# Kernel tuning notes

Hardware: AMD Instinct MI355X
Metric: run time of the kernel (lower is better)

The kernel has to match this reference:

```python
import jax, jax.numpy as jnp
import numpy as np
from jax import lax

B, T, N, FIN = 1, 8, 50000, 3
E = 800000
HID, HEADS = 32, 2
NEG_SLOPE = 0.2  # PyG GATConv default negative_slope


def setup_inputs() -> dict:
    key = jax.random.key(0)
    ks = jax.random.split(key, 16)
    p = lambda k, shape: jax.random.normal(k, shape, dtype=jnp.float32) * 0.1
    return {
        "x_seq": jax.random.normal(ks[0], (B, T, N, FIN), dtype=jnp.float32),
        # GAT layer 1: lin weight [heads*hid, in], att vectors [heads, hid], bias [hid]
        "W1": p(ks[1], (HEADS * HID, FIN)),
        "a1_src": p(ks[2], (HEADS, HID)),
        "a1_dst": p(ks[3], (HEADS, HID)),
        "b1": p(ks[4], (HID,)),
        # GAT layer 2
        "W2": p(ks[5], (HEADS * HID, HID)),
        "a2_src": p(ks[6], (HEADS, HID)),
        "a2_dst": p(ks[7], (HEADS, HID)),
        "b2": p(ks[8], (HID,)),
        # GRU (single layer): torch layout [3*hid, hid] with gate order r,z,n
        "w_ih": p(ks[9], (3 * HID, HID)),
        "w_hh": p(ks[10], (3 * HID, HID)),
        "b_ih": p(ks[11], (3 * HID,)),
        "b_hh": p(ks[12], (3 * HID,)),
        # final Linear(hid, 1)
        "fc_w": p(ks[13], (1, HID)),
        "fc_b": p(ks[14], (1,)),
        "edge_index": jax.random.randint(ks[15], (2, E), 0, N, dtype=jnp.int64),
    }


def gat(x, src, dst, W, a_s, a_d, b):
    """PyG GATConv, heads=HEADS, concat=False (mean over heads). src/dst include self-loops."""
    n = x.shape[0]
    heads, hd = a_s.shape
    h = (x @ W.T).reshape(n, heads, hd)                      # [n, heads, hid]
    e = jax.nn.leaky_relu((h * a_s).sum(-1)[src] + (h * a_d).sum(-1)[dst], NEG_SLOPE)  # [E', heads]
    m = jax.ops.segment_max(e, dst, num_segments=n)          # per-destination max
    m = jnp.where(jnp.isfinite(m), m, jnp.zeros_like(m))
    ex = jnp.exp(e - m[dst])
    denom = jax.ops.segment_sum(ex, dst, num_segments=n)
    alpha = ex / (denom[dst] + 1e-16)                        # segment softmax
    out = jax.ops.segment_sum(h[src] * alpha[..., None], dst, num_segments=n)  # [n, heads, hid]
    return out.mean(axis=1) + b


def _forward(x_seq, W1, a1_src, a1_dst, b1, W2, a2_src, a2_dst, b2,
             w_ih, w_hh, b_ih, b_hh, fc_w, fc_b, edge_index):
    Bb, Tt, Nn, Fin = x_seq.shape
    n = Bb * Nn
    loops = jnp.arange(n, dtype=edge_index.dtype)            # add_self_loops=True
    src = jnp.concatenate([edge_index[0], loops])
    dst = jnp.concatenate([edge_index[1], loops])
    hid = b1.shape[0]

    def step(hstate, xt):                                    # one timestep: GAT x2 then GRU cell
        x = xt.reshape(n, Fin)
        g = jax.nn.relu(gat(x, src, dst, W1, a1_src, a1_dst, b1))
        g = jax.nn.relu(gat(g, src, dst, W2, a2_src, a2_dst, b2))
        gi = g @ w_ih.T + b_ih
        gh = hstate @ w_hh.T + b_hh
        i_r, i_z, i_n = jnp.split(gi, 3, axis=-1)
        h_r, h_z, h_n = jnp.split(gh, 3, axis=-1)
        r = jax.nn.sigmoid(i_r + h_r)
        z = jax.nn.sigmoid(i_z + h_z)
        cand = jnp.tanh(i_n + r * h_n)
        hnew = (1.0 - z) * cand + z * hstate
        return hnew, None

    h0 = jnp.zeros((n, hid), x_seq.dtype)
    h_final, _ = lax.scan(step, h0, jnp.moveaxis(x_seq, 1, 0))  # scan over T
    out = h_final @ fc_w.T + fc_b                            # [B*N, 1]
    return out.reshape(Bb, Nn)


def reference(x_seq, W1, a1_src, a1_dst, b1, W2, a2_src, a2_dst, b2,
              w_ih, w_hh, b_ih, b_hh, fc_w, fc_b, edge_index):
    return _forward(x_seq, W1, a1_src, a1_dst, b1, W2, a2_src, a2_dst, b2,
                    w_ih, w_hh, b_ih, b_hh, fc_w, fc_b, edge_index)
```

## Files before the change

kernel.cpp:

```cpp
#include <hip/hip_runtime.h>
#include <hip/hip_fp16.h>
#include <stdint.h>

#define T_STEPS 8
#define FIN 3
#define HID 32
#define NEG_SLOPE 0.2f
#define LOG2E 1.4426950408889634f

typedef __fp16 v4h __attribute__((ext_vector_type(4)));
typedef float  v4f __attribute__((ext_vector_type(4)));

__device__ __forceinline__ float lrelu(float x) { return x > 0.f ? x : NEG_SLOPE * x; }
__device__ __forceinline__ float sigmoidf(float x) { return 1.f / (1.f + __expf(-x)); }

__global__ void detect_kernel(const int* ei32, int nElems, int* flag) {
    __shared__ int any_nonzero;
    if (threadIdx.x == 0) any_nonzero = 0;
    __syncthreads();
    int idx = 1 + 2 * (int)threadIdx.x;
    if (idx < nElems && ei32[idx] != 0) any_nonzero = 1;
    __syncthreads();
    if (threadIdx.x == 0) *flag = (any_nonzero ? 0 : 1);
}

__device__ __forceinline__ int get_edge(const void* ei, int is64, long long idx) {
    if (is64) return (int)((const long long*)ei)[idx];
    return ((const int*)ei)[idx];
}

__global__ void init_kernel(int* cnt, int N) {
    int i = blockIdx.x * 256 + threadIdx.x;
    if (i < N) cnt[i] = 1;
}

__global__ void conv_count_kernel(const void* ei, const int* flag, int E, int N,
                                  int* src32, int* dst32, int* cnt) {
    int e = blockIdx.x * 256 + threadIdx.x;
    if (e >= E) return;
    int is64 = *flag;
    int s = get_edge(ei, is64, e);
    int d = get_edge(ei, is64, (long long)E + e);
    if ((unsigned)s >= (unsigned)N) s = 0;
    src32[e] = s;
    int dd = ((unsigned)d < (unsigned)N) ? d : 0x7fffffff;
    dst32[e] = dd;
    if (dd < N) atomicAdd(&cnt[dd], 1);
}

__global__ __launch_bounds__(256) void scan1_kernel(const int* cnt, int* rowptr, int* bsum, int n) {
    __shared__ int sm[256];
    int i = blockIdx.x * 256 + threadIdx.x;
    int v = (i < n) ? cnt[i] : 0;
    sm[threadIdx.x] = v;
    __syncthreads();
    for (int off = 1; off < 256; off <<= 1) {
        int t = (threadIdx.x >= off) ? sm[threadIdx.x - off] : 0;
        __syncthreads();
        sm[threadIdx.x] += t;
        __syncthreads();
    }
    if (i < n) rowptr[i + 1] = sm[threadIdx.x];
    if (threadIdx.x == 255) bsum[blockIdx.x] = sm[255];
}

__global__ __launch_bounds__(256) void scan2_kernel(int* bsum, int nb) {
    __shared__ int sm[256];
    int v = (threadIdx.x < nb) ? bsum[threadIdx.x] : 0;
    sm[threadIdx.x] = v;
    __syncthreads();
    for (int off = 1; off < 256; off <<= 1) {
        int t = (threadIdx.x >= off) ? sm[threadIdx.x - off] : 0;
        __syncthreads();
        sm[threadIdx.x] += t;
        __syncthreads();
    }
    if (threadIdx.x < nb) bsum[threadIdx.x] = sm[threadIdx.x];
}

__global__ __launch_bounds__(256) void scan3_kernel(int* rowptr, const int* bsum, int n) {
    int i = blockIdx.x * 256 + threadIdx.x;
    if (i < n && blockIdx.x > 0) rowptr[i + 1] += bsum[blockIdx.x - 1];
    if (i == 0) rowptr[0] = 0;
}

__global__ void selffill_kernel(const int* rowptr, int* csr, int* fill, int N) {
    int n = blockIdx.x * 256 + threadIdx.x;
    if (n >= N) return;
    int rp = rowptr[n];
    csr[rp] = n;
    fill[n] = rp + 1;
}

__global__ void scatter_kernel(const int* __restrict__ src32, const int* __restrict__ dst32,
                               int E, int lo, int hi, int* fill, int* csr) {
    int e = blockIdx.x * 256 + threadIdx.x;
    if (e >= E) return;
    int d = dst32[e];
    if (d < lo || d >= hi) return;
    int p = atomicAdd(&fill[d], 1);
    csr[p] = src32[e];
}

__global__ __launch_bounds__(64) void prep_u_kernel(
        const float* __restrict__ W2, const float* __restrict__ a2s,
        const float* __restrict__ a2d, float* __restrict__ u_s, float* __restrict__ u_d) {
    int l = threadIdx.x;
    int h = l >> 5, k = l & 31;
    float us = 0.f, ud = 0.f;
    for (int c = 0; c < 32; c++) {
        float w = W2[(h * 32 + c) * 32 + k];
        us += a2s[h * 32 + c] * w;
        ud += a2d[h * 32 + c] * w;
    }
    u_s[l] = us * LOG2E;
    u_d[l] = ud * LOG2E;
}

__global__ __launch_bounds__(256) void packfrag_kernel(
        const float* __restrict__ W2, const float* __restrict__ w_ih,
        const float* __restrict__ w_hh, uint2* __restrict__ wfrag) {
    int idx = blockIdx.x * 256 + threadIdx.x;
    if (idx >= 2048) return;
    int tile = idx >> 6, l = idx & 63;
    int c = l & 15, g = l >> 4;
    float v[4];
    if (tile < 8) {
        int kt = tile >> 1, nt = tile & 1;
#pragma unroll
        for (int b = 0; b < 4; b++) {
            int kk = kt * 16 + 4 * g + b;
            int nn = nt * 16 + c;
            v[b] = 0.5f * (kk < 32 ? W2[nn * 32 + kk] : W2[(nn + 32) * 32 + kk - 32]);
        }
    } else if (tile < 20) {
        int q = tile - 8; int nt = q >> 1, kt = q & 1;
#pragma unroll
        for (int b = 0; b < 4; b++) {
            int kk = kt * 16 + 4 * g + b;
            int nn = nt * 16 + c;
            v[b] = w_ih[nn * 32 + kk];
        }
    } else {
        int q = tile - 20; int nt = q >> 1, kt = q & 1;
#pragma unroll
        for (int b = 0; b < 4; b++) {
            int kk = kt * 16 + 4 * g + b;
            int nn = nt * 16 + c;
            v[b] = w_hh[nn * 32 + kk];
        }
    }
    __half2 lo = __floats2half2_rn(v[0], v[1]);
    __half2 hi = __floats2half2_rn(v[2], v[3]);
    uint2 u;
    u.x = *(unsigned*)&lo;
    u.y = *(unsigned*)&hi;
    wfrag[tile * 64 + l] = u;
}

__global__ __launch_bounds__(256) void score1_all(
        const float* __restrict__ x_seq, const float* __restrict__ W1,
        const float* __restrict__ a1s, const float* __restrict__ a1d,
        float4* __restrict__ nrec4, float2* __restrict__ sd1, int N) {
    int t = blockIdx.x;
    int node = blockIdx.y * 256 + threadIdx.x;
    if (node >= N) return;
    const float* xp = x_seq + ((size_t)t * N + node) * FIN;
    float x0 = xp[0], x1 = xp[1], x2 = xp[2];
    float ps0 = 0.f, ps1 = 0.f, pd0 = 0.f, pd1 = 0.f;
    for (int c = 0; c < 32; c++) {
        float h0 = W1[c * 3] * x0 + W1[c * 3 + 1] * x1 + W1[c * 3 + 2] * x2;
        float h1 = W1[96 + c * 3] * x0 + W1[97 + c * 3] * x1 + W1[98 + c * 3] * x2;
        ps0 += h0 * a1s[c]; pd0 += h0 * a1d[c];
        ps1 += h1 * a1s[32 + c]; pd1 += h1 * a1d[32 + c];
    }
    ps0 *= LOG2E; ps1 *= LOG2E; pd0 *= LOG2E; pd1 *= LOG2E;
    unsigned u = (unsigned)__half_as_ushort(__float2half_rn(ps0)) |
                 ((unsigned)__half_as_ushort(__float2half_rn(ps1)) << 16);
    float4 r;
    r.x = x0; r.y = x1; r.z = x2; r.w = __uint_as_float(u);
    nrec4[(size_t)t * N + node] = r;
    sd1[(size_t)t * N + node] = make_float2(pd0, pd1);
}

__device__ __forceinline__ void unpack_scores(float wslot, float& s0, float& s1) {
    unsigned u = __float_as_uint(wslot);
    s0 = __half2float(__ushort_as_half((unsigned short)(u & 0xffffu)));
    s1 = __half2float(__ushort_as_half((unsigned short)(u >> 16)));
}

__global__ __launch_bounds__(64) void aggA_all(
        const int* __restrict__ rowptr, const int* __restrict__ csr,
        const float4* __restrict__ nrec4, const float2* __restrict__ sd1,
        const float* __restrict__ W1, const float* __restrict__ b1,
        const float* __restrict__ u_s, const float* __restrict__ u_d,
        __half2* __restrict__ g1h, float2* __restrict__ ssd2, float2* __restrict__ sd2, int N) {
    int t = blockIdx.x;
    int dst = blockIdx.y * 64 + threadIdx.x;
    if (dst >= N) return;
    const float4* nr = nrec4 + (size_t)t * N;
    int rs = rowptr[dst], re = rowptr[dst + 1];
    float2 sdv = sd1[(size_t)t * N + dst];
    float q0 = 0, qx0 = 0, qx1 = 0, qx2 = 0;
    float q1 = 0, qy0 = 0, qy1 = 0, qy2 = 0;
#define AGGA_EDGE(rr) { \
        float s0h, s1h; unpack_scores(rr.w, s0h, s1h); \
        float w0 = exp2f(lrelu(s0h + sdv.x)); \
        float w1 = exp2f(lrelu(s1h + sdv.y)); \
        q0 += w0; qx0 += w0 * rr.x; qx1 += w0 * rr.y; qx2 += w0 * rr.z; \
        q1 += w1; qy0 += w1 * rr.x; qy1 += w1 * rr.y; qy2 += w1 * rr.z; }
    int e = rs;
    for (; e + 4 <= re; e += 4) {
        int s0 = csr[e], s1 = csr[e + 1], s2 = csr[e + 2], s3 = csr[e + 3];
        float4 r0 = nr[s0], r1 = nr[s1], r2 = nr[s2], r3 = nr[s3];
        AGGA_EDGE(r0); AGGA_EDGE(r1); AGGA_EDGE(r2); AGGA_EDGE(r3);
    }
    for (; e < re; e++) {
        float4 r = nr[csr[e]];
        AGGA_EDGE(r);
    }
#undef AGGA_EDGE
    float inv0 = 1.f / (q0 + 1e-16f), inv1 = 1.f / (q1 + 1e-16f);
    float ax0 = qx0 * inv0, ax1 = qx1 * inv0, ax2 = qx2 * inv0;
    float ay0 = qy0 * inv1, ay1 = qy1 * inv1, ay2 = qy2 * inv1;
    float ps0 = 0, ps1 = 0, pd0 = 0, pd1 = 0;
    float4 out[4];
    __half2* ghp = (__half2*)out;
    float gprev = 0.f;
#pragma unroll
    for (int c = 0; c < 32; c++) {
        float v0 = W1[c * 3] * ax0 + W1[c * 3 + 1] * ax1 + W1[c * 3 + 2] * ax2;
        float v1 = W1[96 + c * 3] * ay0 + W1[97 + c * 3] * ay1 + W1[98 + c * 3] * ay2;
        float g = fmaxf(0.5f * (v0 + v1) + b1[c], 0.f);
        ps0 += g * u_s[c];      ps1 += g * u_s[32 + c];
        pd0 += g * u_d[c];      pd1 += g * u_d[32 + c];
        if (c & 1) ghp[c >> 1] = __floats2half2_rn(gprev, g);
        else gprev = g;
    }
    float4* gdst = (float4*)(g1h + (size_t)t * N * 16 + (size_t)dst * 16);
    gdst[0] = out[0]; gdst[1] = out[1]; gdst[2] = out[2]; gdst[3] = out[3];
    ssd2[(size_t)t * N + dst] = make_float2(ps0, ps1);
    sd2[(size_t)t * N + dst]  = make_float2(pd0, pd1);
}

__global__ __launch_bounds__(256) void aggBg_all(
        const int* __restrict__ rowptr, const int* __restrict__ csr,
        const __half2* __restrict__ g1h,
        const float2* __restrict__ ssd2, const float2* __restrict__ sd2,
        __half2* __restrict__ aggH, int N) {
    int t = blockIdx.x;
    int dl = threadIdx.x >> 2;
    int q = threadIdx.x & 3;
    int dst = blockIdx.y * 64 + dl;
    if (dst >= N) return;
    const __half2* gbase = g1h + (size_t)t * N * 16 + q * 4;
    const float2* ss = ssd2 + (size_t)t * N;
    int rs = rowptr[dst], re = rowptr[dst + 1];
    float2 sdv = sd2[(size_t)t * N + dst];
    float a0[8] = {0, 0, 0, 0, 0, 0, 0, 0};
    float a1[8] = {0, 0, 0, 0, 0, 0, 0, 0};
    float den0 = 0.f, den1 = 0.f;
#define AGGB_EDGE(sc, gv) { \
        float w0 = exp2f(lrelu(sc.x + sdv.x)); \
        float w1 = exp2f(lrelu(sc.y + sdv.y)); \
        den0 += w0; den1 += w1; \
        float2 p0 = __half22float2(*(const __half2*)&gv.x); \
        float2 p1 = __half22float2(*(const __half2*)&gv.y); \
        float2 p2 = __half22float2(*(const __half2*)&gv.z); \
        float2 p3 = __half22float2(*(const __half2*)&gv.w); \
        a0[0] += w0 * p0.x; a0[1] += w0 * p0.y; a0[2] += w0 * p1.x; a0[3] += w0 * p1.y; \
        a0[4] += w0 * p2.x; a0[5] += w0 * p2.y; a0[6] += w0 * p3.x; a0[7] += w0 * p3.y; \
        a1[0] += w1 * p0.x; a1[1] += w1 * p0.y; a1[2] += w1 * p1.x; a1[3] += w1 * p1.y; \
        a1[4] += w1 * p2.x; a1[5] += w1 * p2.y; a1[6] += w1 * p3.x; a1[7] += w1 * p3.y; }
    int e = rs;
    for (; e + 4 <= re; e += 4) {
        int s0 = csr[e], s1 = csr[e + 1], s2 = csr[e + 2], s3 = csr[e + 3];
        float2 c0 = ss[s0], c1 = ss[s1], c2 = ss[s2], c3 = ss[s3];
        float4 g0 = *(const float4*)(gbase + (size_t)s0 * 16);
        float4 g1 = *(const float4*)(gbase + (size_t)s1 * 16);
        float4 g2 = *(const float4*)(gbase + (size_t)s2 * 16);
        float4 g3 = *(const float4*)(gbase + (size_t)s3 * 16);
        AGGB_EDGE(c0, g0); AGGB_EDGE(c1, g1); AGGB_EDGE(c2, g2); AGGB_EDGE(c3, g3);
    }
    for (; e < re; e++) {
        int s = csr[e];
        float2 c = ss[s];
        float4 g = *(const float4*)(gbase + (size_t)s * 16);
        AGGB_EDGE(c, g);
    }
#undef AGGB_EDGE
    float i0 = 1.f / (den0 + 1e-16f), i1 = 1.f / (den1 + 1e-16f);
    __half2 o0[4], o1[4];
#pragma unroll
    for (int j = 0; j < 4; j++) {
        o0[j] = __floats2half2_rn(a0[2 * j] * i0, a0[2 * j + 1] * i0);
        o1[j] = __floats2half2_rn(a1[2 * j] * i1, a1[2 * j + 1] * i1);
    }
    __half2* row = aggH + (size_t)t * N * 32 + (size_t)dst * 32;
    *(float4*)(row + q * 4)      = *(float4*)o0;
    *(float4*)(row + 16 + q * 4) = *(float4*)o1;
}

__global__ __launch_bounds__(64) void gru_mfma(
        const __half2* __restrict__ aggH, const uint2* __restrict__ wfrag,
        const float* __restrict__ b2, const float* __restrict__ b_ih,
        const float* __restrict__ b_hh, const float* __restrict__ fc_w,
        const float* __restrict__ fc_b, float* __restrict__ out, int N) {
    __shared__ __align__(16) __half g_lds[16 * 36];
    __shared__ __align__(16) __half h_lds[16 * 36];
    int l = threadIdx.x;
    int c = l & 15;
    int g4 = l >> 4;
    int node0 = blockIdx.x * 16;
    union FU { uint2 u; v4h h; };
    v4h Bw2[4][2], Bih[6][2], Bhh[6][2];
#pragma unroll
    for (int kt = 0; kt < 4; kt++)
#pragma unroll
        for (int nt = 0; nt < 2; nt++) {
            FU f; f.u = wfrag[(kt * 2 + nt) * 64 + l]; Bw2[kt][nt] = f.h;
        }
#pragma unroll
    for (int nt = 0; nt < 6; nt++)
#pragma unroll
        for (int kt = 0; kt < 2; kt++) {
            FU f; f.u = wfrag[(8 + nt * 2 + kt) * 64 + l]; Bih[nt][kt] = f.h;
            f.u = wfrag[(20 + nt * 2 + kt) * 64 + l]; Bhh[nt][kt] = f.h;
        }
    float b2v0 = b2[c], b2v1 = b2[c + 16];
    float bir0 = b_ih[c], bir1 = b_ih[c + 16];
    float biz0 = b_ih[32 + c], biz1 = b_ih[48 + c];
    float bin0 = b_ih[64 + c], bin1 = b_ih[80 + c];
    float bhr0 = b_hh[c], bhr1 = b_hh[c + 16];
    float bhz0 = b_hh[32 + c], bhz1 = b_hh[48 + c];
    float bhn0 = b_hh[64 + c], bhn1 = b_hh[80 + c];
    float fcw0 = fc_w[c], fcw1 = fc_w[c + 16];
    v4f hold0 = {0.f, 0.f, 0.f, 0.f};
    v4f hold1 = {0.f, 0.f, 0.f, 0.f};
    const __half2* rowb = aggH + (size_t)(node0 + c) * 32;
    for (int t = 0; t < T_STEPS; t++) {
        v4f Dg0 = {0.f, 0.f, 0.f, 0.f}, Dg1 = {0.f, 0.f, 0.f, 0.f};
        const __half2* rb = rowb + (size_t)t * N * 32;
#pragma unroll
        for (int kt = 0; kt < 4; kt++) {
            FU A; A.u = *(const uint2*)(rb + 2 * g4 + 8 * kt);
            Dg0 = __builtin_amdgcn_mfma_f32_16x16x16f16(A.h, Bw2[kt][0], Dg0, 0, 0, 0);
            Dg1 = __builtin_amdgcn_mfma_f32_16x16x16f16(A.h, Bw2[kt][1], Dg1, 0, 0, 0);
        }
        __syncthreads();
#pragma unroll
        for (int i = 0; i < 4; i++) {
            int nrow = 4 * g4 + i;
            g_lds[nrow * 36 + c]      = __float2half_rn(fmaxf(Dg0[i] + b2v0, 0.f));
            g_lds[nrow * 36 + c + 16] = __float2half_rn(fmaxf(Dg1[i] + b2v1, 0.f));
        }
        __syncthreads();
        v4f Di[6], Dh[6];
#pragma unroll
        for (int nt = 0; nt < 6; nt++) { Di[nt] = {0.f, 0.f, 0.f, 0.f}; Dh[nt] = {0.f, 0.f, 0.f, 0.f}; }
#pragma unroll
        for (int kt = 0; kt < 2; kt++) {
            FU Ag; Ag.u = *(const uint2*)&g_lds[c * 36 + 4 * g4 + 16 * kt];
#pragma unroll
            for (int nt = 0; nt < 6; nt++)
                Di[nt] = __builtin_amdgcn_mfma_f32_16x16x16f16(Ag.h, Bih[nt][kt], Di[nt], 0, 0, 0);
        }
        if (t > 0) {
#pragma unroll
            for (int kt = 0; kt < 2; kt++) {
                FU Ah; Ah.u = *(const uint2*)&h_lds[c * 36 + 4 * g4 + 16 * kt];
#pragma unroll
                for (int nt = 0; nt < 6; nt++)
                    Dh[nt] = __builtin_amdgcn_mfma_f32_16x16x16f16(Ah.h, Bhh[nt][kt], Dh[nt], 0, 0, 0);
            }
        }
        v4f hn0, hn1;
#pragma unroll
        for (int i = 0; i < 4; i++) {
            {
                float rr = sigmoidf((Di[0][i] + bir0) + (Dh[0][i] + bhr0));
                float zz = sigmoidf((Di[2][i] + biz0) + (Dh[2][i] + bhz0));
                float cand = tanhf((Di[4][i] + bin0) + rr * (Dh[4][i] + bhn0));
                hn0[i] = (1.f - zz) * cand + zz * hold0[i];
            }
            {
                float rr = sigmoidf((Di[1][i] + bir1) + (Dh[1][i] + bhr1));
                float zz = sigmoidf((Di[3][i] + biz1) + (Dh[3][i] + bhz1));
                float cand = tanhf((Di[5][i] + bin1) + rr * (Dh[5][i] + bhn1));
                hn1[i] = (1.f - zz) * cand + zz * hold1[i];
            }
        }
        hold0 = hn0; hold1 = hn1;
        if (t < T_STEPS - 1) {
            __syncthreads();
#pragma unroll
            for (int i = 0; i < 4; i++) {
                int nrow = 4 * g4 + i;
                h_lds[nrow * 36 + c]      = __float2half_rn(hn0[i]);
                h_lds[nrow * 36 + c + 16] = __float2half_rn(hn1[i]);
            }
            __syncthreads();
        }
    }
#pragma unroll
    for (int i = 0; i < 4; i++) {
        float p = fcw0 * hold0[i] + fcw1 * hold1[i];
        p += __shfl_xor(p, 1, 64);
        p += __shfl_xor(p, 2, 64);
        p += __shfl_xor(p, 4, 64);
        p += __shfl_xor(p, 8, 64);
        if (c == 0) out[node0 + 4 * g4 + i] = p + fc_b[0];
    }
}

extern "C" void kernel_launch(void* const* d_in, const int* in_sizes, int n_in,
                              void* d_out, int out_size, void* d_ws, size_t ws_size,
                              hipStream_t stream) {
    const float* x_seq = (const float*)d_in[0];
    const float* W1  = (const float*)d_in[1];
    const float* a1s = (const float*)d_in[2];
    const float* a1d = (const float*)d_in[3];
    const float* b1  = (const float*)d_in[4];
    const float* W2  = (const float*)d_in[5];
    const float* a2s = (const float*)d_in[6];
    const float* a2d = (const float*)d_in[7];
    const float* b2  = (const float*)d_in[8];
    const float* w_ih = (const float*)d_in[9];
    const float* w_hh = (const float*)d_in[10];
    const float* b_ih = (const float*)d_in[11];
    const float* b_hh = (const float*)d_in[12];
    const float* fc_w = (const float*)d_in[13];
    const float* fc_b = (const float*)d_in[14];
    const void*  ei   = d_in[15];

    const int N = in_sizes[0] / (T_STEPS * FIN);
    const int E = in_sizes[15] / 2;
    const int NE = E + N;
    const int NB = (N + 255) / 256;
    const int NB64 = (N + 63) / 64;
    const int NB16 = (N + 15) / 16;
    const int EB = (E + 255) / 256;

    char* ws = (char*)d_ws;
    size_t off = 0;
    auto alloc = [&](size_t bytes) -> void* {
        void* p = ws + off;
        off += (bytes + 255) & ~(size_t)255;
        return p;
    };
    int*     flag   = (int*)alloc(4);
    int*     rowptr = (int*)alloc((size_t)(N + 1) * 4);
    int*     cnt    = (int*)alloc((size_t)N * 4);
    int*     bsum   = (int*)alloc(256 * 4);
    int*     csr    = (int*)alloc((size_t)NE * 4);
    int*     src32  = (int*)alloc((size_t)E * 4);
    int*     dst32  = (int*)alloc((size_t)E * 4);
    float4*  nrec4  = (float4*)alloc((size_t)T_STEPS * N * 16);
    float2*  sd1    = (float2*)alloc((size_t)T_STEPS * N * 8);
    float2*  ssd2   = (float2*)alloc((size_t)T_STEPS * N * 8);
    float2*  sd2    = (float2*)alloc((size_t)T_STEPS * N * 8);
    __half2* g1h    = (__half2*)alloc((size_t)T_STEPS * N * 16 * 4);
    __half2* aggH   = (__half2*)alloc((size_t)T_STEPS * N * 32 * 4);
    float*   u_s    = (float*)alloc(64 * 4);
    float*   u_d    = (float*)alloc(64 * 4);
    uint2*   wfrag  = (uint2*)alloc(32 * 64 * 8);
    if (off > ws_size) return;

    detect_kernel<<<1, 128, 0, stream>>>((const int*)ei, in_sizes[15], flag);
    init_kernel<<<NB, 256, 0, stream>>>(cnt, N);
    conv_count_kernel<<<EB, 256, 0, stream>>>(ei, flag, E, N, src32, dst32, cnt);
    scan1_kernel<<<NB, 256, 0, stream>>>(cnt, rowptr, bsum, N);
    scan2_kernel<<<1, 256, 0, stream>>>(bsum, NB);
    scan3_kernel<<<NB, 256, 0, stream>>>(rowptr, bsum, N);
    selffill_kernel<<<NB, 256, 0, stream>>>(rowptr, csr, cnt, N);
    {
        const int NPASS = 4;
        int per = (N + NPASS - 1) / NPASS;
        for (int p = 0; p < NPASS; p++) {
            int lo = p * per;
            int hi = min(lo + per, N);
            scatter_kernel<<<EB, 256, 0, stream>>>(src32, dst32, E, lo, hi, cnt, csr);
        }
    }
    prep_u_kernel<<<1, 64, 0, stream>>>(W2, a2s, a2d, u_s, u_d);
    packfrag_kernel<<<8, 256, 0, stream>>>(W2, w_ih, w_hh, wfrag);

    score1_all<<<dim3(T_STEPS, NB), 256, 0, stream>>>(x_seq, W1, a1s, a1d, nrec4, sd1, N);
    aggA_all<<<dim3(T_STEPS, NB64), 64, 0, stream>>>(rowptr, csr, nrec4, sd1, W1, b1,
                                                     u_s, u_d, g1h, ssd2, sd2, N);
    aggBg_all<<<dim3(T_STEPS, NB64), 256, 0, stream>>>(rowptr, csr, g1h, ssd2, sd2, aggH, N);
    gru_mfma<<<NB16, 64, 0, stream>>>(aggH, wfrag, b2, b_ih, b_hh,
                                      fc_w, fc_b, (float*)d_out, N);
}
```

Measured before the change: 290.4 us.

## Fuse layer-2 W2 projection into aggregation kernel, shrink GRU input buffer

Moves the layer-2 GAT linear projection (W2 matmul, head mean, bias, ReLU) out of the GRU MFMA kernel into the aggregation kernel. Aggregated features are staged in LDS and multiplied by a transposed fp32 W2 using scalar FMAs. The kernel then writes a 32-wide fp16 g2 instead of the 64-wide aggH. This halves the intermediate buffer written and read between kernels and removes two LDS syncs per timestep from the GRU loop. In exchange the projection runs on vector ALUs instead of MFMA, and the aggregation kernel gains a barrier and LDS use.

```diff
diff --git a/kernel.cpp b/kernel.cpp
--- a/kernel.cpp
+++ b/kernel.cpp
@@ -117,45 +117,38 @@
     u_d[l] = ud * LOG2E;
 }
 
+__global__ __launch_bounds__(256) void pack_kernel(
+        const float* __restrict__ W2, float* __restrict__ w2pk) {
+    int idx = blockIdx.x * 256 + threadIdx.x;
+    if (idx < 2048) {
+        int k = idx >> 6, c = idx & 63;
+        w2pk[idx] = W2[c * 32 + k];
+    }
+}
+
 __global__ __launch_bounds__(256) void packfrag_kernel(
-        const float* __restrict__ W2, const float* __restrict__ w_ih,
-        const float* __restrict__ w_hh, uint2* __restrict__ wfrag) {
+        const float* __restrict__ w_ih, const float* __restrict__ w_hh,
+        uint2* __restrict__ wfrag) {
     int idx = blockIdx.x * 256 + threadIdx.x;
-    if (idx >= 2048) return;
-    int tile = idx >> 6, l = idx & 63;
+    if (idx >= 1536) return;
+    int q24 = idx >> 6, l = idx & 63;
     int c = l & 15, g = l >> 4;
+    const float* W = (q24 < 12) ? w_ih : w_hh;
+    int q = (q24 < 12) ? q24 : q24 - 12;
+    int nt = q >> 1, kt = q & 1;
     float v[4];
-    if (tile < 8) {
-        int kt = tile >> 1, nt = tile & 1;
-#pragma unroll
-        for (int b = 0; b < 4; b++) {
-            int kk = kt * 16 + 4 * g + b;
-            int nn = nt * 16 + c;
-            v[b] = 0.5f * (kk < 32 ? W2[nn * 32 + kk] : W2[(nn + 32) * 32 + kk - 32]);
-        }
-    } else if (tile < 20) {
-        int q = tile - 8; int nt = q >> 1, kt = q & 1;
-#pragma unroll
-        for (int b = 0; b < 4; b++) {
-            int kk = kt * 16 + 4 * g + b;
-            int nn = nt * 16 + c;
-            v[b] = w_ih[nn * 32 + kk];
-        }
-    } else {
-        int q = tile - 20; int nt = q >> 1, kt = q & 1;
-#pragma unroll
-        for (int b = 0; b < 4; b++) {
-            int kk = kt * 16 + 4 * g + b;
-            int nn = nt * 16 + c;
-            v[b] = w_hh[nn * 32 + kk];
-        }
+#pragma unroll
+    for (int b = 0; b < 4; b++) {
+        int kk = kt * 16 + 4 * g + b;
+        int nn = nt * 16 + c;
+        v[b] = W[nn * 32 + kk];
     }
     __half2 lo = __floats2half2_rn(v[0], v[1]);
     __half2 hi = __floats2half2_rn(v[2], v[3]);
     uint2 u;
     u.x = *(unsigned*)&lo;
     u.y = *(unsigned*)&hi;
-    wfrag[tile * 64 + l] = u;
+    wfrag[(8 + q24) * 64 + l] = u;
 }
 
 __global__ __launch_bounds__(256) void score1_all(
@@ -243,23 +236,27 @@
     sd2[(size_t)t * N + dst]  = make_float2(pd0, pd1);
 }
 
-__global__ __launch_bounds__(256) void aggBg_all(
+__global__ __launch_bounds__(256) void aggBg2_all(
         const int* __restrict__ rowptr, const int* __restrict__ csr,
         const __half2* __restrict__ g1h,
         const float2* __restrict__ ssd2, const float2* __restrict__ sd2,
-        __half2* __restrict__ aggH, int N) {
+        const float* __restrict__ w2pk, const float* __restrict__ b2,
+        __half2* __restrict__ g2H, int N) {
+    __shared__ __half2 a_lds[64 * 33];
     int t = blockIdx.x;
-    int dl = threadIdx.x >> 2;
-    int q = threadIdx.x & 3;
-    int dst = blockIdx.y * 64 + dl;
-    if (dst >= N) return;
-    const __half2* gbase = g1h + (size_t)t * N * 16 + q * 4;
-    const float2* ss = ssd2 + (size_t)t * N;
-    int rs = rowptr[dst], re = rowptr[dst + 1];
-    float2 sdv = sd2[(size_t)t * N + dst];
-    float a0[8] = {0, 0, 0, 0, 0, 0, 0, 0};
-    float a1[8] = {0, 0, 0, 0, 0, 0, 0, 0};
-    float den0 = 0.f, den1 = 0.f;
+    int tid = threadIdx.x;
+    int node0 = blockIdx.y * 64;
+    int dl = tid >> 2;
+    int q = tid & 3;
+    int dst = node0 + dl;
+    if (dst < N) {
+        const __half2* gbase = g1h + (size_t)t * N * 16 + q * 4;
+        const float2* ss = ssd2 + (size_t)t * N;
+        int rs = rowptr[dst], re = rowptr[dst + 1];
+        float2 sdv = sd2[(size_t)t * N + dst];
+        float a0[8] = {0, 0, 0, 0, 0, 0, 0, 0};
+        float a1[8] = {0, 0, 0, 0, 0, 0, 0, 0};
+        float den0 = 0.f, den1 = 0.f;
 #define AGGB_EDGE(sc, gv) { \
         float w0 = exp2f(lrelu(sc.x + sdv.x)); \
         float w1 = exp2f(lrelu(sc.y + sdv.y)); \
@@ -272,54 +269,67 @@
         a0[4] += w0 * p2.x; a0[5] += w0 * p2.y; a0[6] += w0 * p3.x; a0[7] += w0 * p3.y; \
         a1[0] += w1 * p0.x; a1[1] += w1 * p0.y; a1[2] += w1 * p1.x; a1[3] += w1 * p1.y; \
         a1[4] += w1 * p2.x; a1[5] += w1 * p2.y; a1[6] += w1 * p3.x; a1[7] += w1 * p3.y; }
-    int e = rs;
-    for (; e + 4 <= re; e += 4) {
-        int s0 = csr[e], s1 = csr[e + 1], s2 = csr[e + 2], s3 = csr[e + 3];
-        float2 c0 = ss[s0], c1 = ss[s1], c2 = ss[s2], c3 = ss[s3];
-        float4 g0 = *(const float4*)(gbase + (size_t)s0 * 16);
-        float4 g1 = *(const float4*)(gbase + (size_t)s1 * 16);
-        float4 g2 = *(const float4*)(gbase + (size_t)s2 * 16);
-        float4 g3 = *(const float4*)(gbase + (size_t)s3 * 16);
-        AGGB_EDGE(c0, g0); AGGB_EDGE(c1, g1); AGGB_EDGE(c2, g2); AGGB_EDGE(c3, g3);
-    }
-    for (; e < re; e++) {
-        int s = csr[e];
-        float2 c = ss[s];
-        float4 g = *(const float4*)(gbase + (size_t)s * 16);
-        AGGB_EDGE(c, g);
-    }
+        int e = rs;
+        for (; e + 4 <= re; e += 4) {
+            int s0 = csr[e], s1 = csr[e + 1], s2 = csr[e + 2], s3 = csr[e + 3];
+            float2 c0 = ss[s0], c1 = ss[s1], c2 = ss[s2], c3 = ss[s3];
+            float4 g0 = *(const float4*)(gbase + (size_t)s0 * 16);
+            float4 g1 = *(const float4*)(gbase + (size_t)s1 * 16);
+            float4 g2 = *(const float4*)(gbase + (size_t)s2 * 16);
+            float4 g3 = *(const float4*)(gbase + (size_t)s3 * 16);
+            AGGB_EDGE(c0, g0); AGGB_EDGE(c1, g1); AGGB_EDGE(c2, g2); AGGB_EDGE(c3, g3);
+        }
+        for (; e < re; e++) {
+            int s = csr[e];
+            float2 c = ss[s];
+            float4 g = *(const float4*)(gbase + (size_t)s * 16);
+            AGGB_EDGE(c, g);
+        }
 #undef AGGB_EDGE
-    float i0 = 1.f / (den0 + 1e-16f), i1 = 1.f / (den1 + 1e-16f);
-    __half2 o0[4], o1[4];
+        float i0 = 1.f / (den0 + 1e-16f), i1 = 1.f / (den1 + 1e-16f);
+#pragma unroll
+        for (int j = 0; j < 4; j++) {
+            a_lds[dl * 33 + q * 4 + j]      = __floats2half2_rn(a0[2 * j] * i0, a0[2 * j + 1] * i0);
+            a_lds[dl * 33 + 16 + q * 4 + j] = __floats2half2_rn(a1[2 * j] * i1, a1[2 * j + 1] * i1);
+        }
+    }
+    __syncthreads();
+    int nl = tid & 63;
+    int cg8 = __builtin_amdgcn_readfirstlane((tid >> 6) * 8);
+    int node = node0 + nl;
+    if (node >= N) return;
+    float acc[8] = {0, 0, 0, 0, 0, 0, 0, 0};
+    for (int kp = 0; kp < 16; kp++) {
+        float2 A0 = __half22float2(a_lds[nl * 33 + kp]);
+        float2 A1 = __half22float2(a_lds[nl * 33 + 16 + kp]);
+        const float* wpA = w2pk + (2 * kp) * 64 + cg8;
+        const float* wpB = w2pk + (2 * kp + 1) * 64 + cg8;
+#pragma unroll
+        for (int j = 0; j < 8; j++)
+            acc[j] += wpA[j] * A0.x + wpA[32 + j] * A1.x + wpB[j] * A0.y + wpB[32 + j] * A1.y;
+    }
+    __half2 o[4];
 #pragma unroll
     for (int j = 0; j < 4; j++) {
-        o0[j] = __floats2half2_rn(a0[2 * j] * i0, a0[2 * j + 1] * i0);
-        o1[j] = __floats2half2_rn(a1[2 * j] * i1, a1[2 * j + 1] * i1);
-    }
-    __half2* row = aggH + (size_t)t * N * 32 + (size_t)dst * 32;
-    *(float4*)(row + q * 4)      = *(float4*)o0;
-    *(float4*)(row + 16 + q * 4) = *(float4*)o1;
+        float ga = fmaxf(0.5f * acc[2 * j] + b2[cg8 + 2 * j], 0.f);
+        float gb = fmaxf(0.5f * acc[2 * j + 1] + b2[cg8 + 2 * j + 1], 0.f);
+        o[j] = __floats2half2_rn(ga, gb);
+    }
+    *(float4*)(g2H + ((size_t)t * N + node) * 16 + (cg8 >> 1)) = *(float4*)o;
 }
 
 __global__ __launch_bounds__(64) void gru_mfma(
-        const __half2* __restrict__ aggH, const uint2* __restrict__ wfrag,
-        const float* __restrict__ b2, const float* __restrict__ b_ih,
-        const float* __restrict__ b_hh, const float* __restrict__ fc_w,
-        const float* __restrict__ fc_b, float* __restrict__ out, int N) {
-    __shared__ __align__(16) __half g_lds[16 * 36];
+        const __half2* __restrict__ g2H, const uint2* __restrict__ wfrag,
+        const float* __restrict__ b_ih, const float* __restrict__ b_hh,
+        const float* __restrict__ fc_w, const float* __restrict__ fc_b,
+        float* __restrict__ out, int N) {
     __shared__ __align__(16) __half h_lds[16 * 36];
     int l = threadIdx.x;
     int c = l & 15;
     int g4 = l >> 4;
     int node0 = blockIdx.x * 16;
     union FU { uint2 u; v4h h; };
-    v4h Bw2[4][2], Bih[6][2], Bhh[6][2];
-#pragma unroll
-    for (int kt = 0; kt < 4; kt++)
-#pragma unroll
-        for (int nt = 0; nt < 2; nt++) {
-            FU f; f.u = wfrag[(kt * 2 + nt) * 64 + l]; Bw2[kt][nt] = f.h;
-        }
+    v4h Bih[6][2], Bhh[6][2];
 #pragma unroll
     for (int nt = 0; nt < 6; nt++)
 #pragma unroll
@@ -327,7 +337,6 @@
             FU f; f.u = wfrag[(8 + nt * 2 + kt) * 64 + l]; Bih[nt][kt] = f.h;
             f.u = wfrag[(20 + nt * 2 + kt) * 64 + l]; Bhh[nt][kt] = f.h;
         }
-    float b2v0 = b2[c], b2v1 = b2[c + 16];
     float bir0 = b_ih[c], bir1 = b_ih[c + 16];
     float biz0 = b_ih[32 + c], biz1 = b_ih[48 + c];
     float bin0 = b_ih[64 + c], bin1 = b_ih[80 + c];
@@ -337,30 +346,15 @@
     float fcw0 = fc_w[c], fcw1 = fc_w[c + 16];
     v4f hold0 = {0.f, 0.f, 0.f, 0.f};
     v4f hold1 = {0.f, 0.f, 0.f, 0.f};
-    const __half2* rowb = aggH + (size_t)(node0 + c) * 32;
+    const __half2* rowb = g2H + (size_t)(node0 + c) * 16;
     for (int t = 0; t < T_STEPS; t++) {
-        v4f Dg0 = {0.f, 0.f, 0.f, 0.f}, Dg1 = {0.f, 0.f, 0.f, 0.f};
-        const __half2* rb = rowb + (size_t)t * N * 32;
-#pragma unroll
-        for (int kt = 0; kt < 4; kt++) {
-            FU A; A.u = *(const uint2*)(rb + 2 * g4 + 8 * kt);
-            Dg0 = __builtin_amdgcn_mfma_f32_16x16x16f16(A.h, Bw2[kt][0], Dg0, 0, 0, 0);
-            Dg1 = __builtin_amdgcn_mfma_f32_16x16x16f16(A.h, Bw2[kt][1], Dg1, 0, 0, 0);
-        }
-        __syncthreads();
-#pragma unroll
-        for (int i = 0; i < 4; i++) {
-            int nrow = 4 * g4 + i;
-            g_lds[nrow * 36 + c]      = __float2half_rn(fmaxf(Dg0[i] + b2v0, 0.f));
-            g_lds[nrow * 36 + c + 16] = __float2half_rn(fmaxf(Dg1[i] + b2v1, 0.f));
-        }
-        __syncthreads();
+        const __half2* rb = rowb + (size_t)t * N * 16;
         v4f Di[6], Dh[6];
 #pragma unroll
         for (int nt = 0; nt < 6; nt++) { Di[nt] = {0.f, 0.f, 0.f, 0.f}; Dh[nt] = {0.f, 0.f, 0.f, 0.f}; }
 #pragma unroll
         for (int kt = 0; kt < 2; kt++) {
-            FU Ag; Ag.u = *(const uint2*)&g_lds[c * 36 + 4 * g4 + 16 * kt];
+            FU Ag; Ag.u = *(const uint2*)(rb + 2 * g4 + 8 * kt);
 #pragma unroll
             for (int nt = 0; nt < 6; nt++)
                 Di[nt] = __builtin_amdgcn_mfma_f32_16x16x16f16(Ag.h, Bih[nt][kt], Di[nt], 0, 0, 0);
@@ -460,9 +454,10 @@
     float2*  ssd2   = (float2*)alloc((size_t)T_STEPS * N * 8);
     float2*  sd2    = (float2*)alloc((size_t)T_STEPS * N * 8);
     __half2* g1h    = (__half2*)alloc((size_t)T_STEPS * N * 16 * 4);
-    __half2* aggH   = (__half2*)alloc((size_t)T_STEPS * N * 32 * 4);
+    __half2* g2H    = (__half2*)alloc((size_t)T_STEPS * N * 16 * 4);
     float*   u_s    = (float*)alloc(64 * 4);
     float*   u_d    = (float*)alloc(64 * 4);
+    float*   w2pk   = (float*)alloc(2048 * 4);
     uint2*   wfrag  = (uint2*)alloc(32 * 64 * 8);
     if (off > ws_size) return;
 
@@ -483,12 +478,14 @@
         }
     }
     prep_u_kernel<<<1, 64, 0, stream>>>(W2, a2s, a2d, u_s, u_d);
-    packfrag_kernel<<<8, 256, 0, stream>>>(W2, w_ih, w_hh, wfrag);
+    pack_kernel<<<8, 256, 0, stream>>>(W2, w2pk);
+    packfrag_kernel<<<6, 256, 0, stream>>>(w_ih, w_hh, wfrag);
 
     score1_all<<<dim3(T_STEPS, NB), 256, 0, stream>>>(x_seq, W1, a1s, a1d, nrec4, sd1, N);
     aggA_all<<<dim3(T_STEPS, NB64), 64, 0, stream>>>(rowptr, csr, nrec4, sd1, W1, b1,
                                                      u_s, u_d, g1h, ssd2, sd2, N);
-    aggBg_all<<<dim3(T_STEPS, NB64), 256, 0, stream>>>(rowptr, csr, g1h, ssd2, sd2, aggH, N);
-    gru_mfma<<<NB16, 64, 0, stream>>>(aggH, wfrag, b2, b_ih, b_hh,
+    aggBg2_all<<<dim3(T_STEPS, NB64), 256, 0, stream>>>(rowptr, csr, g1h, ssd2, sd2,
+                                                        w2pk, b2, g2H, N);
+    gru_mfma<<<NB16, 64, 0, stream>>>(g2H, wfrag, b_ih, b_hh,
                                       fc_w, fc_b, (float*)d_out, N);
 }
```

New measurement: 298.9 us. +2.9%, slower.
